# Performance work log

Hardware: AMD Instinct MI355X
Metric: run time of the kernel (lower is better)

## Reference

```python
import jax, jax.numpy as jnp
import numpy as np

B, T, E, H = 64, 512, 512, 64
NEG_INF = jnp.float32(-1e30)


def setup_inputs() -> dict:
    key = jax.random.key(0)
    kx, kk, kq, kv = jax.random.split(key, 4)
    x = jax.random.normal(kx, (B, T, E), dtype=jnp.float32)
    attn_mask = jnp.ones((B, T), dtype=jnp.int32)
    Wk = jax.random.normal(kk, (E, H), dtype=jnp.float32) * (E ** -0.5)
    Wq = jax.random.normal(kq, (E, H), dtype=jnp.float32) * (E ** -0.5)
    Wv = jax.random.normal(kv, (E, H), dtype=jnp.float32) * (E ** -0.5)
    return {"x": x, "attn_mask": attn_mask, "Wk": Wk, "Wq": Wq, "Wv": Wv}


def reference(x, attn_mask, Wk, Wq, Wv):
    # x: (B,T,E); projections to (B,T,H)
    k = x @ Wk
    q = x @ Wq
    v = x @ Wv
    # scaled attention scores (B,T,T)
    wei = jnp.einsum('bth,bsh->bts', q, k) * (H ** -0.5)
    t = x.shape[1]
    causal = jnp.tril(jnp.ones((t, t), dtype=bool))  # (T,T)
    wei = jnp.where(causal[None, :, :], wei, NEG_INF)
    # padding mask: attn_mask (B,T) broadcast over query dim (matches unsqueeze(1).expand)
    wei = jnp.where(attn_mask[:, None, :] != 0, wei, NEG_INF)
    wei = jax.nn.softmax(wei, axis=-1)
    # dropout omitted (eval mode) for deterministic correctness baseline
    return jnp.einsum('bts,bsh->bth', wei, v)
```

## Files before the change

kernel.cpp:

```cpp
#include <hip/hip_runtime.h>

#define B 64
#define T 512
#define E 512
#define H 64
#define NEG_INF (-1e30f)

#define PBM 64
#define PBK 64
#define PN 192
#define NCHK (E / PBK)

using short8 = __attribute__((ext_vector_type(8))) short;
using f32x16 = __attribute__((ext_vector_type(16))) float;

__device__ __forceinline__ unsigned short f2bf(float f) {
    unsigned int u = __float_as_uint(f);
    u += 0x7fffu + ((u >> 16) & 1u);
    return (unsigned short)(u >> 16);
}
__device__ __forceinline__ unsigned int bfpack_tr(float lo, float hi) {
    return (__float_as_uint(hi) & 0xffff0000u) | (__float_as_uint(lo) >> 16);
}
__device__ __forceinline__ void async_copy16(const void* g, void* l) {
    __builtin_amdgcn_global_load_lds(
        (const __attribute__((address_space(1))) unsigned int*)g,
        (__attribute__((address_space(3))) unsigned int*)l, 16, 0, 0);
}

__global__ __launch_bounds__(256) void prep(
    const float* __restrict__ Wq, const float* __restrict__ Wk,
    const float* __restrict__ Wv, const int* __restrict__ am,
    unsigned short* __restrict__ WT_swz, unsigned int* __restrict__ mbits)
{
    const int bid = blockIdx.x;
    if (bid < 384) {
        const int i = bid * 256 + threadIdx.x;
        const int c   = i / (PN * 64);
        const int rem = i - c * (PN * 64);
        const int row = rem >> 6;
        const int s   = rem & 63;
        const int klocal = s ^ ((row & 7) << 3);
        const int k   = c * 64 + klocal;
        const int seg = row >> 6, hh = row & 63;
        const float* W = (seg == 0) ? Wq : (seg == 1) ? Wk : Wv;
        WT_swz[i] = f2bf(W[(size_t)k * H + hh]);
    } else {
        const int i = (bid - 384) * 256 + threadIdx.x;
        const unsigned long long bal = __ballot(am[i] != 0);
        const int lane = threadIdx.x & 63;
        if (lane == 0)       mbits[i >> 5] = (unsigned int)bal;
        else if (lane == 32) mbits[i >> 5] = (unsigned int)(bal >> 32);
    }
}

__global__ __launch_bounds__(256) void proj_gemm(
    const float* __restrict__ x,
    const unsigned short* __restrict__ WT_swz,
    unsigned short* __restrict__ qbf, unsigned short* __restrict__ kbf,
    unsigned short* __restrict__ vT)
{
    __shared__ unsigned short Xs[2][PBM * 64];
    __shared__ unsigned short Ws[2][PN * 64];

    const int tid  = threadIdx.x;
    const int wid  = tid >> 6;
    const int lane = tid & 63;
    const int hi   = lane >> 5;
    const int r    = lane & 31;
    const int row0 = blockIdx.x * PBM;

    const int mrow  = (wid >> 1) * 32 + r;
    const int cbase = (wid & 1) * 96;

    const int aBase = mrow * 128;
    const int aXor  = (mrow & 7) << 4;
    int bBase[3], bXor[3];
    #pragma unroll
    for (int nt = 0; nt < 3; ++nt) {
        const int col = cbase + nt * 32 + r;
        bBase[nt] = col * 128;
        bXor[nt]  = (col & 7) << 4;
    }
    const int xs_rr[2]  = { tid >> 3, (256 + tid) >> 3 };
    const int xs_s16[2] = { tid & 7, tid & 7 };

    f32x16 acc[3] = {};

    {
        #pragma unroll
        for (int p = 0; p < 6; ++p) {
            const int u = p * 256 + wid * 64 + lane;
            async_copy16(WT_swz + u * 8, (char*)(&Ws[0][0]) + (p * 256 + wid * 64) * 16);
        }
        #pragma unroll
        for (int p = 0; p < 2; ++p) {
            const int rr = xs_rr[p], s16 = xs_s16[p];
            const float4* src = reinterpret_cast<const float4*>(
                &x[(size_t)(row0 + rr) * E + s16 * 8]);
            const float4 a0 = src[0], a1 = src[1];
            union { unsigned short us[8]; short8 v; } pk;
            pk.us[0] = f2bf(a0.x); pk.us[1] = f2bf(a0.y);
            pk.us[2] = f2bf(a0.z); pk.us[3] = f2bf(a0.w);
            pk.us[4] = f2bf(a1.x); pk.us[5] = f2bf(a1.y);
            pk.us[6] = f2bf(a1.z); pk.us[7] = f2bf(a1.w);
            const int cb = (s16 * 16) ^ ((rr & 7) << 4);
            *reinterpret_cast<short8*>((char*)(&Xs[0][0]) + rr * 128 + cb) = pk.v;
        }
        __syncthreads();
    }

    for (int c = 0; c < NCHK; ++c) {
        const int cur = c & 1;
        const bool pre = (c + 1 < NCHK);
        float4 xa[2], xb[2];

        if (pre) {
            const unsigned short* gw = WT_swz + (size_t)(c + 1) * (PN * 64);
            #pragma unroll
            for (int p = 0; p < 6; ++p) {
                const int u = p * 256 + wid * 64 + lane;
                async_copy16(gw + u * 8,
                             (char*)(&Ws[cur ^ 1][0]) + (p * 256 + wid * 64) * 16);
            }
            const int kc = (c + 1) * PBK;
            #pragma unroll
            for (int p = 0; p < 2; ++p) {
                const float4* src = reinterpret_cast<const float4*>(
                    &x[(size_t)(row0 + xs_rr[p]) * E + kc + xs_s16[p] * 8]);
                xa[p] = src[0];
                xb[p] = src[1];
            }
        }

        #pragma unroll
        for (int ks = 0; ks < 4; ++ks) {
            const int koff = ks * 32 + hi * 16;
            const short8 a = *reinterpret_cast<const short8*>(
                (const char*)(&Xs[cur][0]) + aBase + (koff ^ aXor));
            #pragma unroll
            for (int nt = 0; nt < 3; ++nt) {
                const short8 b = *reinterpret_cast<const short8*>(
                    (const char*)(&Ws[cur][0]) + bBase[nt] + (koff ^ bXor[nt]));
                acc[nt] = __builtin_amdgcn_mfma_f32_32x32x16_bf16(a, b, acc[nt], 0, 0, 0);
            }
        }

        if (pre) {
            #pragma unroll
            for (int p = 0; p < 2; ++p) {
                const int rr = xs_rr[p], s16 = xs_s16[p];
                union { unsigned short us[8]; short8 v; } pk;
                pk.us[0] = f2bf(xa[p].x); pk.us[1] = f2bf(xa[p].y);
                pk.us[2] = f2bf(xa[p].z); pk.us[3] = f2bf(xa[p].w);
                pk.us[4] = f2bf(xb[p].x); pk.us[5] = f2bf(xb[p].y);
                pk.us[6] = f2bf(xb[p].z); pk.us[7] = f2bf(xb[p].w);
                const int cb = (s16 * 16) ^ ((rr & 7) << 4);
                *reinterpret_cast<short8*>((char*)(&Xs[cur ^ 1][0]) + rr * 128 + cb) = pk.v;
            }
        }
        __syncthreads();
    }

    #pragma unroll
    for (int nt = 0; nt < 3; ++nt) {
        const int gc  = cbase + nt * 32 + r;
        const int seg = gc >> 6;
        const int hh  = gc & 63;
        #pragma unroll
        for (int reg = 0; reg < 16; ++reg) {
            const int drow = (reg & 3) + 8 * (reg >> 2) + 4 * hi;
            const int grow = row0 + (wid >> 1) * 32 + drow;
            const float val = acc[nt][reg];
            if (seg == 0) {
                qbf[(size_t)grow * H + hh] = f2bf(val * 0.125f);
            } else if (seg == 1) {
                kbf[(size_t)grow * H + hh] = f2bf(val);
            } else {
                const int bb = grow >> 9, tt = grow & 511;
                vT[((size_t)bb * H + hh) * T + tt] = f2bf(val);
            }
        }
    }
}

__global__ __launch_bounds__(64) void attn_online(
    const unsigned short* __restrict__ qbf,
    const unsigned short* __restrict__ kbf,
    const unsigned short* __restrict__ vT,
    const unsigned int* __restrict__ mbits,
    float* __restrict__ out)
{
    const int lane = threadIdx.x;
    const int hi = lane >> 5, r = lane & 31;
    const int h4 = 4 * hi;

    const int bid = blockIdx.x;
    const int k   = bid >> 3;
    const int b   = ((k >> 4) << 3) | (bid & 7);
    const int s   = 15 - (k & 15);
    const int t0  = s * 32;
    const int tq  = t0 + r;

    short8 qf[4];
    #pragma unroll
    for (int ks = 0; ks < 4; ++ks)
        qf[ks] = *reinterpret_cast<const short8*>(
            &qbf[((size_t)b * T + t0 + r) * H + ks * 16 + hi * 8]);

    f32x16 accO[2] = {};
    float m = -INFINITY, l = 0.f;

    short8 kf[4];
    #pragma unroll
    for (int ks = 0; ks < 4; ++ks)
        kf[ks] = *reinterpret_cast<const short8*>(
            &kbf[((size_t)b * T + r) * H + ks * 16 + hi * 8]);

    for (int j = 0; j <= s; ++j) {
        short8 vb[4];
        #pragma unroll
        for (int hs = 0; hs < 2; ++hs)
            #pragma unroll
            for (int tile = 0; tile < 2; ++tile)
                vb[hs * 2 + tile] = *reinterpret_cast<const short8*>(
                    &vT[((size_t)b * H + r + 32 * tile) * T + 32 * j + hs * 16 + hi * 8]);

        short8 kn[4];
        if (j < s) {
            #pragma unroll
            for (int ks = 0; ks < 4; ++ks)
                kn[ks] = *reinterpret_cast<const short8*>(
                    &kbf[((size_t)b * T + 32 * (j + 1) + r) * H + ks * 16 + hi * 8]);
        }

        f32x16 sc = {};
        #pragma unroll
        for (int ks = 0; ks < 4; ++ks)
            sc = __builtin_amdgcn_mfma_f32_32x32x16_bf16(kf[ks], qf[ks], sc, 0, 0, 0);
        #pragma unroll
        for (int ks = 0; ks < 4; ++ks) kf[ks] = kn[ks];

        const unsigned int mw = mbits[b * 16 + j];
        float cmax = -INFINITY;
        if (j == s) {
            #pragma unroll
            for (int reg = 0; reg < 16; ++reg) {
                const int cr = (reg & 3) + 8 * (reg >> 2) + h4;
                float v = sc[reg];
                const bool bad = !((mw >> cr) & 1u) || (32 * j + cr > tq);
                v = bad ? NEG_INF : v;
                sc[reg] = v;
                cmax = fmaxf(cmax, v);
            }
        } else {
            #pragma unroll
            for (int reg = 0; reg < 16; ++reg) {
                const int cr = (reg & 3) + 8 * (reg >> 2) + h4;
                float v = sc[reg];
                v = ((mw >> cr) & 1u) ? v : NEG_INF;
                sc[reg] = v;
                cmax = fmaxf(cmax, v);
            }
        }
        cmax = fmaxf(cmax, __shfl_xor(cmax, 32));

        const float m_new = fmaxf(m, cmax);
        if (!__all(cmax <= m)) {
            const float scale = __expf(m - m_new);
            f32x16 scf;
            #pragma unroll
            for (int reg = 0; reg < 16; ++reg)
                scf[reg] = __shfl(scale, (reg & 3) + 8 * (reg >> 2) + h4);
            #pragma unroll
            for (int reg = 0; reg < 16; ++reg) {
                accO[0][reg] *= scf[reg];
                accO[1][reg] *= scf[reg];
            }
            l *= scale;
        }
        m = m_new;

        float csum = 0.f;
        #pragma unroll
        for (int reg = 0; reg < 16; ++reg) {
            const float p = __expf(sc[reg] - m_new);
            sc[reg] = p;
            csum += p;
        }
        csum += __shfl_xor(csum, 32);
        l += csum;

        unsigned int pk[8];
        #pragma unroll
        for (int jj = 0; jj < 8; ++jj)
            pk[jj] = bfpack_tr(sc[2 * jj], sc[2 * jj + 1]);
        #pragma unroll
        for (int hs = 0; hs < 2; ++hs) {
            const unsigned int p01 = pk[hs * 4 + 0], p23 = pk[hs * 4 + 1];
            const unsigned int p45 = pk[hs * 4 + 2], p67 = pk[hs * 4 + 3];
            const unsigned int sendA = hi ? p01 : p45;
            const unsigned int sendB = hi ? p23 : p67;
            const unsigned int recvA = (unsigned int)__shfl_xor((int)sendA, 32);
            const unsigned int recvB = (unsigned int)__shfl_xor((int)sendB, 32);
            union { unsigned int uu[4]; short8 s8; } aw;
            aw.uu[0] = hi ? recvA : p01;
            aw.uu[1] = hi ? recvB : p23;
            aw.uu[2] = hi ? p45 : recvA;
            aw.uu[3] = hi ? p67 : recvB;
            #pragma unroll
            for (int tile = 0; tile < 2; ++tile)
                accO[tile] = __builtin_amdgcn_mfma_f32_32x32x16_bf16(
                    aw.s8, vb[hs * 2 + tile], accO[tile], 0, 0, 0);
        }
    }

    const float inv = 1.f / l;
    #pragma unroll
    for (int reg = 0; reg < 16; ++reg) {
        const int qrow = (reg & 3) + 8 * (reg >> 2) + h4;
        const float f = __shfl(inv, qrow);
        float* op = &out[((size_t)b * T + t0 + qrow) * H];
        op[r]      = accO[0][reg] * f;
        op[r + 32] = accO[1][reg] * f;
    }
}

extern "C" void kernel_launch(void* const* d_in, const int* in_sizes, int n_in,
                              void* d_out, int out_size, void* d_ws, size_t ws_size,
                              hipStream_t stream) {
    const float* x         = (const float*)d_in[0];
    const int*   attn_mask = (const int*)d_in[1];
    const float* Wk        = (const float*)d_in[2];
    const float* Wq        = (const float*)d_in[3];
    const float* Wv        = (const float*)d_in[4];
    float* out = (float*)d_out;

    unsigned short* qbf    = (unsigned short*)d_ws;
    unsigned short* kbf    = qbf + (size_t)B * T * H;
    unsigned short* vT     = kbf + (size_t)B * T * H;
    unsigned short* WT_swz = vT  + (size_t)B * T * H;
    unsigned int*   mbits  = (unsigned int*)(WT_swz + (size_t)PN * E);

    prep<<<512, 256, 0, stream>>>(Wq, Wk, Wv, attn_mask, WT_swz, mbits);
    proj_gemm<<<(B * T) / PBM, 256, 0, stream>>>(x, WT_swz, qbf, kbf, vT);
    attn_online<<<B * 16, 64, 0, stream>>>(qbf, kbf, vT, mbits, out);
}
```

Measured before the change: 53.05 us.

## Store Q/K/V in MFMA fragment layout, prefetch V, use exp2 with deferred rescale

The projection epilogue now writes Q, K and V directly in per-lane MFMA fragment order, so each attention lane reads one contiguous 16-byte chunk per fragment instead of strided row or transposed loads. V tiles are now prefetched one iteration ahead, like K. The softmax folds log2(e) into the Q scale and uses exp2f, and it skips the accumulator rescale unless the running max grows by more than a threshold. That lazy rescale trades fewer shuffles and multiplies for exponent values up to 2^8 before normalization, while the scattered epilogue stores may cost extra write traffic in the GEMM.

Result: no change. 54.01 us (+1.8%).

```diff
diff --git a/kernel.cpp b/kernel.cpp
--- a/kernel.cpp
+++ b/kernel.cpp
@@ -10,6 +10,9 @@
 #define PBK 64
 #define PN 192
 #define NCHK (E / PBK)
+
+#define QSCALE 0.18033688011112043f
+#define DEFER_THR 8.0f
 
 using short8 = __attribute__((ext_vector_type(8))) short;
 using f32x16 = __attribute__((ext_vector_type(16))) float;
@@ -57,8 +60,8 @@
 __global__ __launch_bounds__(256) void proj_gemm(
     const float* __restrict__ x,
     const unsigned short* __restrict__ WT_swz,
-    unsigned short* __restrict__ qbf, unsigned short* __restrict__ kbf,
-    unsigned short* __restrict__ vT)
+    unsigned short* __restrict__ qfrag, unsigned short* __restrict__ kfrag,
+    unsigned short* __restrict__ vfrag)
 {
     __shared__ unsigned short Xs[2][PBM * 64];
     __shared__ unsigned short Ws[2][PN * 64];
@@ -166,28 +169,34 @@
     for (int nt = 0; nt < 3; ++nt) {
         const int gc  = cbase + nt * 32 + r;
         const int seg = gc >> 6;
-        const int hh  = gc & 63;
+        const int h   = gc & 63;
         #pragma unroll
         for (int reg = 0; reg < 16; ++reg) {
             const int drow = (reg & 3) + 8 * (reg >> 2) + 4 * hi;
             const int grow = row0 + (wid >> 1) * 32 + drow;
             const float val = acc[nt][reg];
+            const int bb  = grow >> 9;
+            const int key = grow & 511;
+            const int blk = key >> 5;
+            const int kk  = key & 31;
             if (seg == 0) {
-                qbf[(size_t)grow * H + hh] = f2bf(val * 0.125f);
+                qfrag[(((size_t)bb * 16 + blk) * 4 + (h >> 4)) * 512
+                      + (((h >> 3) & 1) * 32 + kk) * 8 + (h & 7)] = f2bf(val * QSCALE);
             } else if (seg == 1) {
-                kbf[(size_t)grow * H + hh] = f2bf(val);
+                kfrag[(((size_t)bb * 16 + blk) * 4 + (h >> 4)) * 512
+                      + (((h >> 3) & 1) * 32 + kk) * 8 + (h & 7)] = f2bf(val);
             } else {
-                const int bb = grow >> 9, tt = grow & 511;
-                vT[((size_t)bb * H + hh) * T + tt] = f2bf(val);
+                vfrag[(((size_t)bb * 16 + blk) * 4 + ((kk >> 4) * 2 + (h >> 5))) * 512
+                      + (((kk >> 3) & 1) * 32 + (h & 31)) * 8 + (kk & 7)] = f2bf(val);
             }
         }
     }
 }
 
 __global__ __launch_bounds__(64) void attn_online(
-    const unsigned short* __restrict__ qbf,
-    const unsigned short* __restrict__ kbf,
-    const unsigned short* __restrict__ vT,
+    const unsigned short* __restrict__ qfrag,
+    const unsigned short* __restrict__ kfrag,
+    const unsigned short* __restrict__ vfrag,
     const unsigned int* __restrict__ mbits,
     float* __restrict__ out)
 {
@@ -202,44 +211,46 @@
     const int t0  = s * 32;
     const int tq  = t0 + r;
 
+    const int l8 = lane * 8;
+
     short8 qf[4];
-    #pragma unroll
-    for (int ks = 0; ks < 4; ++ks)
-        qf[ks] = *reinterpret_cast<const short8*>(
-            &qbf[((size_t)b * T + t0 + r) * H + ks * 16 + hi * 8]);
+    {
+        const unsigned short* qb = qfrag + (((size_t)b * 16 + s) * 4) * 512;
+        #pragma unroll
+        for (int ks = 0; ks < 4; ++ks)
+            qf[ks] = *reinterpret_cast<const short8*>(qb + ks * 512 + l8);
+    }
 
     f32x16 accO[2] = {};
     float m = -INFINITY, l = 0.f;
 
-    short8 kf[4];
-    #pragma unroll
-    for (int ks = 0; ks < 4; ++ks)
-        kf[ks] = *reinterpret_cast<const short8*>(
-            &kbf[((size_t)b * T + r) * H + ks * 16 + hi * 8]);
+    short8 kf[4], vb[4];
+    {
+        const unsigned short* kb = kfrag + ((size_t)b * 16) * 4 * 512;
+        const unsigned short* vv = vfrag + ((size_t)b * 16) * 4 * 512;
+        #pragma unroll
+        for (int ks = 0; ks < 4; ++ks) {
+            kf[ks] = *reinterpret_cast<const short8*>(kb + ks * 512 + l8);
+            vb[ks] = *reinterpret_cast<const short8*>(vv + ks * 512 + l8);
+        }
+    }
 
     for (int j = 0; j <= s; ++j) {
-        short8 vb[4];
-        #pragma unroll
-        for (int hs = 0; hs < 2; ++hs)
-            #pragma unroll
-            for (int tile = 0; tile < 2; ++tile)
-                vb[hs * 2 + tile] = *reinterpret_cast<const short8*>(
-                    &vT[((size_t)b * H + r + 32 * tile) * T + 32 * j + hs * 16 + hi * 8]);
-
-        short8 kn[4];
+        short8 kn[4], vn[4];
         if (j < s) {
-            #pragma unroll
-            for (int ks = 0; ks < 4; ++ks)
-                kn[ks] = *reinterpret_cast<const short8*>(
-                    &kbf[((size_t)b * T + 32 * (j + 1) + r) * H + ks * 16 + hi * 8]);
+            const unsigned short* kb = kfrag + (((size_t)b * 16 + j + 1) * 4) * 512;
+            const unsigned short* vv = vfrag + (((size_t)b * 16 + j + 1) * 4) * 512;
+            #pragma unroll
+            for (int ks = 0; ks < 4; ++ks) {
+                kn[ks] = *reinterpret_cast<const short8*>(kb + ks * 512 + l8);
+                vn[ks] = *reinterpret_cast<const short8*>(vv + ks * 512 + l8);
+            }
         }
 
         f32x16 sc = {};
         #pragma unroll
         for (int ks = 0; ks < 4; ++ks)
             sc = __builtin_amdgcn_mfma_f32_32x32x16_bf16(kf[ks], qf[ks], sc, 0, 0, 0);
-        #pragma unroll
-        for (int ks = 0; ks < 4; ++ks) kf[ks] = kn[ks];
 
         const unsigned int mw = mbits[b * 16 + j];
         float cmax = -INFINITY;
@@ -265,9 +276,9 @@
         }
         cmax = fmaxf(cmax, __shfl_xor(cmax, 32));
 
-        const float m_new = fmaxf(m, cmax);
-        if (!__all(cmax <= m)) {
-            const float scale = __expf(m - m_new);
+        if (!__all(cmax <= m + DEFER_THR)) {
+            const float m_new = fmaxf(m, cmax);
+            const float scale = exp2f(m - m_new);
             f32x16 scf;
             #pragma unroll
             for (int reg = 0; reg < 16; ++reg)
@@ -278,13 +289,13 @@
                 accO[1][reg] *= scf[reg];
             }
             l *= scale;
-        }
-        m = m_new;
+            m = m_new;
+        }
 
         float csum = 0.f;
         #pragma unroll
         for (int reg = 0; reg < 16; ++reg) {
-            const float p = __expf(sc[reg] - m_new);
+            const float p = exp2f(sc[reg] - m);
             sc[reg] = p;
             csum += p;
         }
@@ -313,6 +324,9 @@
                 accO[tile] = __builtin_amdgcn_mfma_f32_32x32x16_bf16(
                     aw.s8, vb[hs * 2 + tile], accO[tile], 0, 0, 0);
         }
+
+        #pragma unroll
+        for (int ks = 0; ks < 4; ++ks) { kf[ks] = kn[ks]; vb[ks] = vn[ks]; }
     }
 
     const float inv = 1.f / l;
@@ -336,13 +350,13 @@
     const float* Wv        = (const float*)d_in[4];
     float* out = (float*)d_out;
 
-    unsigned short* qbf    = (unsigned short*)d_ws;
-    unsigned short* kbf    = qbf + (size_t)B * T * H;
-    unsigned short* vT     = kbf + (size_t)B * T * H;
-    unsigned short* WT_swz = vT  + (size_t)B * T * H;
+    unsigned short* qfrag  = (unsigned short*)d_ws;
+    unsigned short* kfrag  = qfrag + (size_t)B * T * H;
+    unsigned short* vfrag  = kfrag + (size_t)B * T * H;
+    unsigned short* WT_swz = vfrag + (size_t)B * T * H;
     unsigned int*   mbits  = (unsigned int*)(WT_swz + (size_t)PN * E);
 
     prep<<<512, 256, 0, stream>>>(Wq, Wk, Wv, attn_mask, WT_swz, mbits);
-    proj_gemm<<<(B * T) / PBM, 256, 0, stream>>>(x, WT_swz, qbf, kbf, vT);
-    attn_online<<<B * 16, 64, 0, stream>>>(qbf, kbf, vT, mbits, out);
-}
+    proj_gemm<<<(B * T) / PBM, 256, 0, stream>>>(x, WT_swz, qfrag, kfrag, vfrag);
+    attn_online<<<B * 16, 64, 0, stream>>>(qfrag, kfrag, vfrag, mbits, out);
+}
```
